# Kernel optimization log

Hardware: AMD Instinct MI355X
Metric: run time of the kernel (lower is better)

## Reference

```python
import jax, jax.numpy as jnp
import numpy as np

B, H, W = 256, 512, 512
KH, KW = 16, 16
OH, OW = 8, 8
N = (H // KH) * (W // KW)  # 1024 chunks
KIN = KH * KW              # 256
KOUT = OH * OW             # 64


def setup_inputs() -> dict:
    key = jax.random.key(0)
    kx, kw, kb = jax.random.split(key, 3)
    x = jax.random.normal(kx, (B, H, W), dtype=jnp.float32)
    # Per-chunk Linear weights, torch-style uniform(-1/sqrt(fan_in), 1/sqrt(fan_in))
    bound = 1.0 / np.sqrt(KIN)
    Wk = jax.random.uniform(kw, (N, KOUT, KIN), dtype=jnp.float32, minval=-bound, maxval=bound)
    bk = jax.random.uniform(kb, (N, KOUT), dtype=jnp.float32, minval=-bound, maxval=bound)
    return {"x": x, "Wk": Wk, "bk": bk}


def _split_chunks(x):
    # [B,H,W] -> [B, N, KH, KW] matching split_matrix_in_chunks
    b = x.shape[0]
    return (x.reshape(b, H // KH, KH, W // KW, KW)
             .swapaxes(2, 3)
             .reshape(b, N, KH, KW))


def _recombine(chunks):
    # [B, N, OH, OW] -> [B, s*OH, s*OW] matching recombine_chunks_into_matrix
    b = chunks.shape[0]
    s = int(np.sqrt(N))
    return (chunks.reshape(b, s, s, OH, OW)
                  .swapaxes(3, 2)
                  .reshape(b, s * OH, s * OW))


def reference(x, Wk, bk):
    xc = _split_chunks(x).reshape(-1, N, KIN)          # [B,N,KIN]
    # grouped GEMM: one Linear per chunk, fused with bias + ReLU
    y = jnp.einsum('bnk,nok->bno', xc, Wk) + bk[None]  # [B,N,KOUT]
    y = jax.nn.relu(y)
    out = _recombine(y.reshape(-1, N, OH, OW))         # [B, s*OH, s*OW]
    b, h, w = out.shape
    return out.reshape(b, h * w)
```

## Files before the change

kernel.cpp:

```cpp
#include <hip/hip_runtime.h>


typedef __bf16 bf16x8 __attribute__((ext_vector_type(8)));
typedef float  f32x4  __attribute__((ext_vector_type(4)));

constexpr int LDW = 264;

union bfpack {
  unsigned short s[8];
  bf16x8 v;
};

__device__ __forceinline__ unsigned short f2bf(float f) {
  union { float f; unsigned u; } v; v.f = f;
  unsigned r = v.u + 0x7fffu + ((v.u >> 16) & 1u);
  return (unsigned short)(r >> 16);
}

__global__ __launch_bounds__(256, 4) void comp_kernel(
    const float* __restrict__ x, const float* __restrict__ Wk,
    const float* __restrict__ bk, float* __restrict__ out) {
  __shared__ unsigned short Ws[64 * LDW];
  __shared__ float bs[64];

  const int bid = blockIdx.x;
  const int n  = ((bid & 7) << 7) | (bid >> 3);
  const int ci = n >> 5, cj = n & 31;
  const int t = threadIdx.x;
  const int wave = t >> 6, lane = t & 63;
  const int m15 = lane & 15, quad = lane >> 4;

  const float4* wsrc = (const float4*)(Wk + (size_t)n * (64 * 256));
  #pragma unroll
  for (int it = 0; it < 8; ++it) {
    int i2 = it * 512 + t * 2;
    float4 g0 = wsrc[i2];
    float4 g1 = wsrc[i2 + 1];
    int o = i2 >> 6, pos = (i2 & 63) * 4;
    bfpack p;
    p.s[0] = f2bf(g0.x); p.s[1] = f2bf(g0.y); p.s[2] = f2bf(g0.z); p.s[3] = f2bf(g0.w);
    p.s[4] = f2bf(g1.x); p.s[5] = f2bf(g1.y); p.s[6] = f2bf(g1.z); p.s[7] = f2bf(g1.w);
    *(bf16x8*)&Ws[o * LDW + pos] = p.v;
  }
  if (t < 64) bs[t] = bk[n * 64 + t];
  __syncthreads();

  const float* xb = x + (size_t)(ci * 16) * 512 + cj * 16
                      + (quad >> 1) * 512 + (quad & 1) * 8;

  for (int bp = 0; bp < 4; ++bp) {
    const int btile = bp * 64 + wave * 16;
    const float* xp = xb + (size_t)(btile + m15) * (512 * 512);

    float4 v0[8], v1[8];
    #pragma unroll
    for (int ks = 0; ks < 8; ++ks) {
      v0[ks] = *(const float4*)(xp + ks * 1024);
      v1[ks] = *(const float4*)(xp + ks * 1024 + 4);
    }
    __builtin_amdgcn_sched_barrier(0);

    f32x4 acc[4] = {{0,0,0,0},{0,0,0,0},{0,0,0,0},{0,0,0,0}};

    #pragma unroll
    for (int ks = 0; ks < 8; ++ks) {
      bfpack a;
      a.s[0] = f2bf(v0[ks].x); a.s[1] = f2bf(v0[ks].y);
      a.s[2] = f2bf(v0[ks].z); a.s[3] = f2bf(v0[ks].w);
      a.s[4] = f2bf(v1[ks].x); a.s[5] = f2bf(v1[ks].y);
      a.s[6] = f2bf(v1[ks].z); a.s[7] = f2bf(v1[ks].w);

      const int ka = ks * 32 + quad * 8;
      bf16x8 bb[4];
      #pragma unroll
      for (int nt = 0; nt < 4; ++nt)
        bb[nt] = *(const bf16x8*)&Ws[(nt * 16 + m15) * LDW + ka];
      #pragma unroll
      for (int nt = 0; nt < 4; ++nt)
        acc[nt] = __builtin_amdgcn_mfma_f32_16x16x32_bf16(bb[nt], a.v, acc[nt], 0, 0, 0);
    }

    float* op = out + (size_t)(btile + m15) * 65536
                    + (size_t)(ci * 8) * 256 + cj * 8;
    #pragma unroll
    for (int nt = 0; nt < 4; ++nt) {
      const int o0 = nt * 16 + quad * 4;
      float4 b4 = *(const float4*)&bs[o0];
      float4 res;
      res.x = fmaxf(acc[nt][0] + b4.x, 0.f);
      res.y = fmaxf(acc[nt][1] + b4.y, 0.f);
      res.z = fmaxf(acc[nt][2] + b4.z, 0.f);
      res.w = fmaxf(acc[nt][3] + b4.w, 0.f);
      *(float4*)&op[(o0 >> 3) * 256 + (o0 & 7)] = res;
    }
  }
}

extern "C" void kernel_launch(void* const* d_in, const int* in_sizes, int n_in,
                              void* d_out, int out_size, void* d_ws, size_t ws_size,
                              hipStream_t stream) {
  const float* x  = (const float*)d_in[0];
  const float* Wk = (const float*)d_in[1];
  const float* bk = (const float*)d_in[2];
  float* out = (float*)d_out;
  comp_kernel<<<dim3(1024), dim3(256), 0, stream>>>(x, Wk, bk, out);
}
```

Before: 461.6 us.

## Stream x tiles into LDS via async global_load_lds with double buffering

Replaces per-thread register loads of x with direct global-to-LDS async loads (global_load_lds) into a per-wave double-buffered, XOR-swizzled LDS staging area. Loads for the next stage are issued while MFMAs run on the current stage, with explicit vmcnt waits. This is meant to overlap memory latency with compute and cut register pressure. In exchange it adds about 32KB of LDS per block, and launch bounds drop occupancy from 4 to 2 blocks. The hand-counted vmcnt waits are fragile.

```diff
diff --git a/kernel.cpp b/kernel.cpp
--- a/kernel.cpp
+++ b/kernel.cpp
@@ -6,10 +6,7 @@
 
 constexpr int LDW = 264;
 
-union bfpack {
-  unsigned short s[8];
-  bf16x8 v;
-};
+union bfpack { unsigned short s[8]; bf16x8 v; };
 
 __device__ __forceinline__ unsigned short f2bf(float f) {
   union { float f; unsigned u; } v; v.f = f;
@@ -17,11 +14,15 @@
   return (unsigned short)(r >> 16);
 }
 
-__global__ __launch_bounds__(256, 4) void comp_kernel(
+typedef __attribute__((address_space(1))) const void GV;
+typedef __attribute__((address_space(3))) void LV;
+
+__global__ __launch_bounds__(256, 2) void comp_kernel(
     const float* __restrict__ x, const float* __restrict__ Wk,
     const float* __restrict__ bk, float* __restrict__ out) {
   __shared__ unsigned short Ws[64 * LDW];
   __shared__ float bs[64];
+  __shared__ __align__(16) float Xs[4][2][1024];
 
   const int bid = blockIdx.x;
   const int n  = ((bid & 7) << 7) | (bid >> 3);
@@ -29,6 +30,27 @@
   const int t = threadIdx.x;
   const int wave = t >> 6, lane = t & 63;
   const int m15 = lane & 15, quad = lane >> 4;
+
+  const char* xbase = (const char*)x + (size_t)ci * 32768 + (size_t)cj * 64;
+  const int b_hi = lane >> 4;
+  const int rr = (lane & 15) * 16;
+
+  auto stage_issue = [&](int s) {
+    const int bp = s >> 2, q = s & 3;
+    const int btile = bp * 64 + wave * 16;
+    float* dst = &Xs[wave][s & 1][0];
+    #pragma unroll
+    for (int i = 0; i < 4; ++i) {
+      const int b_it = i * 4 + b_hi;
+      const int ro = rr ^ ((b_it & 7) << 4);
+      const char* src = xbase + (size_t)(btile + b_it) * 1048576
+                      + (size_t)((q * 4 + (ro >> 6)) * 2048 + (ro & 63));
+      __builtin_amdgcn_global_load_lds((GV*)src, (LV*)(dst + i * 256), 16, 0, 0);
+    }
+  };
+
+  stage_issue(0);
+  stage_issue(1);
 
   const float4* wsrc = (const float4*)(Wk + (size_t)n * (64 * 256));
   #pragma unroll
@@ -45,39 +67,45 @@
   if (t < 64) bs[t] = bk[n * 64 + t];
   __syncthreads();
 
-  const float* xb = x + (size_t)(ci * 16) * 512 + cj * 16
-                      + (quad >> 1) * 512 + (quad & 1) * 8;
-
+  #pragma unroll
   for (int bp = 0; bp < 4; ++bp) {
     const int btile = bp * 64 + wave * 16;
-    const float* xp = xb + (size_t)(btile + m15) * (512 * 512);
-
-    float4 v0[8], v1[8];
-    #pragma unroll
-    for (int ks = 0; ks < 8; ++ks) {
-      v0[ks] = *(const float4*)(xp + ks * 1024);
-      v1[ks] = *(const float4*)(xp + ks * 1024 + 4);
-    }
-    __builtin_amdgcn_sched_barrier(0);
-
     f32x4 acc[4] = {{0,0,0,0},{0,0,0,0},{0,0,0,0},{0,0,0,0}};
 
     #pragma unroll
-    for (int ks = 0; ks < 8; ++ks) {
-      bfpack a;
-      a.s[0] = f2bf(v0[ks].x); a.s[1] = f2bf(v0[ks].y);
-      a.s[2] = f2bf(v0[ks].z); a.s[3] = f2bf(v0[ks].w);
-      a.s[4] = f2bf(v1[ks].x); a.s[5] = f2bf(v1[ks].y);
-      a.s[6] = f2bf(v1[ks].z); a.s[7] = f2bf(v1[ks].w);
+    for (int q = 0; q < 4; ++q) {
+      const int s = bp * 4 + q;
+      if (s == 15)              asm volatile("s_waitcnt vmcnt(0)" ::: "memory");
+      else if (s >= 4 && q < 2) asm volatile("s_waitcnt vmcnt(8)" ::: "memory");
+      else                      asm volatile("s_waitcnt vmcnt(4)" ::: "memory");
+      __builtin_amdgcn_sched_barrier(0);
 
-      const int ka = ks * 32 + quad * 8;
-      bf16x8 bb[4];
+      const char* Xb = (const char*)&Xs[wave][s & 1][0];
+      const int sw = (m15 & 7) << 4;
       #pragma unroll
-      for (int nt = 0; nt < 4; ++nt)
-        bb[nt] = *(const bf16x8*)&Ws[(nt * 16 + m15) * LDW + ka];
-      #pragma unroll
-      for (int nt = 0; nt < 4; ++nt)
-        acc[nt] = __builtin_amdgcn_mfma_f32_16x16x32_bf16(bb[nt], a.v, acc[nt], 0, 0, 0);
+      for (int ksl = 0; ksl < 2; ++ksl) {
+        const int c = ksl * 128 + quad * 32;
+        float4 v0 = *(const float4*)(Xb + m15 * 256 + ((c)      ^ sw));
+        float4 v1 = *(const float4*)(Xb + m15 * 256 + ((c + 16) ^ sw));
+        bfpack a;
+        a.s[0] = f2bf(v0.x); a.s[1] = f2bf(v0.y); a.s[2] = f2bf(v0.z); a.s[3] = f2bf(v0.w);
+        a.s[4] = f2bf(v1.x); a.s[5] = f2bf(v1.y); a.s[6] = f2bf(v1.z); a.s[7] = f2bf(v1.w);
+
+        const int ka = (q * 2 + ksl) * 32 + quad * 8;
+        bf16x8 bb[4];
+        #pragma unroll
+        for (int nt = 0; nt < 4; ++nt)
+          bb[nt] = *(const bf16x8*)&Ws[(nt * 16 + m15) * LDW + ka];
+        #pragma unroll
+        for (int nt = 0; nt < 4; ++nt)
+          acc[nt] = __builtin_amdgcn_mfma_f32_16x16x32_bf16(bb[nt], a.v, acc[nt], 0, 0, 0);
+      }
+
+      if (s + 2 < 16) {
+        __builtin_amdgcn_sched_barrier(0);
+        stage_issue(s + 2);
+        __builtin_amdgcn_sched_barrier(0);
+      }
     }
 
     float* op = out + (size_t)(btile + m15) * 65536
```

New measurement: 443.2 us. -4.0%, faster.
